# Kernel optimization log

Measured on AMD Instinct MI355X. Metric: run time of the kernel, lower is better.

## Reference

```python
import jax, jax.numpy as jnp
import numpy as np

D_MODEL = 1024
NUM_HEADS = 16
D_K = D_MODEL // NUM_HEADS  # 64


def setup_inputs() -> dict:
    key = jax.random.key(0)
    k1, k2, k3, k4, k5 = jax.random.split(key, 5)
    scale = 1.0 / np.sqrt(D_MODEL)
    x = jax.random.normal(k1, (2, 8192, D_MODEL), dtype=jnp.float32)
    W_qkv = jax.random.normal(k2, (D_MODEL, 3 * D_MODEL), dtype=jnp.float32) * scale
    b_qkv = jax.random.normal(k3, (3 * D_MODEL,), dtype=jnp.float32) * 0.01
    W_out = jax.random.normal(k4, (D_MODEL, D_MODEL), dtype=jnp.float32) * scale
    b_out = jax.random.normal(k5, (D_MODEL,), dtype=jnp.float32) * 0.01
    return {"x": x, "W_qkv": W_qkv, "b_qkv": b_qkv, "W_out": W_out, "b_out": b_out}


def reference(x, W_qkv, b_qkv, W_out, b_out):
    B, S, _ = x.shape
    # qkv: [B, S, 3*d_model] -> reshape [B, S, H, 3*d_k] (matches torch reshape:
    # head h owns contiguous slice [h*3dk:(h+1)*3dk], split into q/k/v of d_k each)
    qkv = (jnp.einsum('bsd,de->bse', x, W_qkv) + b_qkv).reshape(B, S, NUM_HEADS, 3 * D_K)
    q, k, v = qkv[..., :D_K], qkv[..., D_K:2 * D_K], qkv[..., 2 * D_K:]
    # NOTE: faithful to source — no head transpose, so matmul contracts d_k and
    # produces scores across the HEAD axis: [B, S, H, H]
    scores = jnp.einsum('bshd,bsgd->bshg', q, k) / np.sqrt(D_K)
    attn = jax.nn.softmax(scores, axis=-1)  # softmax over heads (g)
    context = jnp.einsum('bshg,bsgd->bshd', attn, v).reshape(B, S, NUM_HEADS * D_K)
    return jnp.einsum('bsd,de->bse', context, W_out) + b_out
```

## Files before the change

kernel.cpp:

```cpp
#include <hip/hip_runtime.h>
#include <hip/hip_bf16.h>

typedef short bf16x8 __attribute__((ext_vector_type(8)));
typedef float f32x4 __attribute__((ext_vector_type(4)));
typedef ushort ushort8_t __attribute__((ext_vector_type(8)));

__device__ __forceinline__ float bf2f(ushort u) {
    union { unsigned int i; float f; } c; c.i = ((unsigned int)u) << 16; return c.f;
}
__device__ __forceinline__ ushort f2bf(float f) {
    union { float f; unsigned int i; } c; c.f = f;
    unsigned int x = c.i;
    return (ushort)((x + 0x7fffu + ((x >> 16) & 1u)) >> 16);
}

#define GLOAD_LDS16(g, l) __builtin_amdgcn_global_load_lds( \
    (const __attribute__((address_space(1))) unsigned int*)(g), \
    (__attribute__((address_space(3))) unsigned int*)(l), 16, 0, 0)

__device__ __forceinline__ void transpose_cvt_body(const float* __restrict__ in,
                                                   ushort* __restrict__ out,
                                                   int K, int N, int bx, int by,
                                                   int tid, float (*tile)[33]) {
    int n0 = bx * 32, k0 = by * 32;
    int tx = tid & 31, ty = tid >> 5;
    #pragma unroll
    for (int i = 0; i < 32; i += 8)
        tile[ty + i][tx] = in[(size_t)(k0 + ty + i) * N + n0 + tx];
    __syncthreads();
    #pragma unroll
    for (int i = 0; i < 32; i += 8)
        out[(size_t)(n0 + ty + i) * K + k0 + tx] = f2bf(tile[tx][ty + i]);
}

__global__ __launch_bounds__(256) void k_prep(const float* __restrict__ x,
                                              ushort* __restrict__ xb,
                                              const float* __restrict__ Wq,
                                              ushort* __restrict__ wqkT,
                                              const float* __restrict__ Wo,
                                              ushort* __restrict__ woT) {
    __shared__ float tile[32][33];
    const int b = blockIdx.x, tid = threadIdx.x;
    if (b < 16384) {
        int i = b * 256 + tid;
        float4 v = ((const float4*)x)[i];
        ushort4 o;
        o.x = f2bf(v.x); o.y = f2bf(v.y); o.z = f2bf(v.z); o.w = f2bf(v.w);
        ((ushort4*)xb)[i] = o;
    } else if (b < 16384 + 3072) {
        int idx = b - 16384;
        transpose_cvt_body(Wq, wqkT, 1024, 3072, idx % 96, idx / 96, tid, tile);
    } else {
        int idx = b - (16384 + 3072);
        transpose_cvt_body(Wo, woT, 1024, 1024, idx & 31, idx >> 5, tid, tile);
    }
}


#define LDSA(c,kk) (lds + (c)*65536 + (kk)*16384)
#define LDSB(c,kk) (lds + (c)*65536 + 32768 + (kk)*16384)
#define STAGE_A(c,kk,col) do { \
    GLOAD_LDS16(gA0 + (col), LDSA(c,kk) + wave*1024); \
    GLOAD_LDS16(gA1 + (col), LDSA(c,kk) + 8192 + wave*1024); } while(0)
#define STAGE_B(c,kk,col) do { \
    GLOAD_LDS16(gB0 + (col), LDSB(c,kk) + wave*1024); \
    GLOAD_LDS16(gB1 + (col), LDSB(c,kk) + 8192 + wave*1024); } while(0)
#define READ_A8(c,kk) do { const char* _p = LDSA(c,kk) + aoff; \
    _Pragma("unroll") for (int m = 0; m < 8; ++m) af[m] = *(const bf16x8*)(_p + m*1024); } while(0)
#define READ_B2(c,kk,n0) do { const char* _p = LDSB(c,kk) + boff; \
    bfr[n0] = *(const bf16x8*)(_p + (n0)*1024); \
    bfr[(n0)+1] = *(const bf16x8*)(_p + ((n0)+1)*1024); } while(0)
#define MF16(n0) do { __builtin_amdgcn_s_setprio(1); \
    _Pragma("unroll") for (int m = 0; m < 8; ++m) { \
    acc[m][n0]     = __builtin_amdgcn_mfma_f32_16x16x32_bf16(af[m], bfr[n0],     acc[m][n0],     0,0,0); \
    acc[m][(n0)+1] = __builtin_amdgcn_mfma_f32_16x16x32_bf16(af[m], bfr[(n0)+1], acc[m][(n0)+1], 0,0,0); } \
    __builtin_amdgcn_s_setprio(0); } while(0)

#define BAR __builtin_amdgcn_s_barrier()
#define SB0 __builtin_amdgcn_sched_barrier(0)
#define VM10 asm volatile("s_waitcnt vmcnt(10)")
#define VM0  asm volatile("s_waitcnt vmcnt(0)")

#define PH1(reads, stage, mf, vm) do { reads; stage; mf; SB0; vm; BAR; SB0; } while(0)

#define ITERX(kb, LAST) do { \
   PH1( { READ_A8(0,0); READ_B2(0,0,0); }, STAGE_B(1,1,(kb)+96),              MF16(0), ); \
   PH1( { READ_B2(0,0,2); },               if(!(LAST)) STAGE_A(0,0,(kb)+128), MF16(2), if(LAST) VM0; else VM10 ); \
   PH1( { READ_A8(0,1); READ_B2(0,1,0); }, if(!(LAST)) STAGE_B(0,0,(kb)+128), MF16(0), ); \
   PH1( { READ_B2(0,1,2); },               if(!(LAST)) STAGE_A(0,1,(kb)+160), MF16(2), if(!(LAST)) VM10 ); \
   PH1( { READ_A8(1,0); READ_B2(1,0,0); }, if(!(LAST)) STAGE_B(0,1,(kb)+160), MF16(0), ); \
   PH1( { READ_B2(1,0,2); },               if(!(LAST)) STAGE_A(1,0,(kb)+192), MF16(2), if(!(LAST)) VM10 ); \
   PH1( { READ_A8(1,1); READ_B2(1,1,0); }, if(!(LAST)) STAGE_B(1,0,(kb)+192), MF16(0), ); \
   PH1( { READ_B2(1,1,2); },               if(!(LAST)) STAGE_A(1,1,(kb)+224), MF16(2), if(!(LAST)) VM10 ); \
} while(0)

template<bool OUT_BF16>
__global__ __launch_bounds__(512, 2) void k_gemm256(const ushort* __restrict__ A,
                                                    const ushort* __restrict__ Bt,
                                                    const float* __restrict__ bias,
                                                    void* __restrict__ Cout,
                                                    int N, int NTN) {
    __shared__ __align__(16) char lds[131072];
    const int K = 1024;
    const int tid = threadIdx.x;
    const int wave = tid >> 6, lane = tid & 63;
    const int wr = wave >> 2, wc = wave & 3;
    const int r = lane & 15, q = lane >> 4;

    const int cpx = gridDim.x >> 3, wg = blockIdx.x;
    const int swz = (wg & 7) * cpx + (wg >> 3);
    const int tm = swz / NTN, tn = swz - tm * NTN;
    const int bm = tm * 256, bn = tn * 256;

    const int srow = tid >> 2;
    const int c16l = (tid & 3) ^ ((srow >> 1) & 3);
    const ushort* gA0 = A  + (size_t)(bm + srow) * K + c16l * 8;
    const ushort* gA1 = gA0 + (size_t)128 * K;
    const ushort* gB0 = Bt + (size_t)(bn + srow) * K + c16l * 8;
    const ushort* gB1 = gB0 + (size_t)128 * K;

    const int chunkx = ((q ^ ((r >> 1) & 3)) << 4);
    const int aoff = (wr * 128 + r) * 64 + chunkx;
    const int boff = (wc * 64 + r) * 64 + chunkx;

    f32x4 acc[8][4];
    #pragma unroll
    for (int m = 0; m < 8; ++m)
        #pragma unroll
        for (int n = 0; n < 4; ++n)
            acc[m][n] = (f32x4){0.f, 0.f, 0.f, 0.f};
    bf16x8 af[8], bfr[4];

    STAGE_A(0,0,0);  STAGE_B(0,0,0);
    STAGE_A(0,1,32); STAGE_B(0,1,32);
    STAGE_A(1,0,64); STAGE_B(1,0,64);
    STAGE_A(1,1,96);
    VM10; BAR; SB0;

    #pragma unroll 1
    for (int i = 0; i < 7; ++i) { ITERX(i * 128, 0); }
    ITERX(896, 1);

    float* Cf = (float*)Cout;
    ushort* Cb = (ushort*)Cout;
    #pragma unroll
    for (int m = 0; m < 8; ++m) {
        int row0 = bm + wr * 128 + m * 16 + q * 4;
        #pragma unroll
        for (int n = 0; n < 4; ++n) {
            int col = bn + wc * 64 + n * 16 + r;
            float bv = bias[col];
            #pragma unroll
            for (int j = 0; j < 4; ++j) {
                float v = acc[m][n][j] + bv;
                if (OUT_BF16) Cb[(size_t)(row0 + j) * N + col] = f2bf(v);
                else          Cf[(size_t)(row0 + j) * N + col] = v;
            }
        }
    }
}

__global__ __launch_bounds__(256) void k_attn_mfma(const ushort* __restrict__ qkv,
                                                   ushort* __restrict__ ctx) {
    __shared__ __align__(16) ushort vlds[4][1024];
    __shared__ __align__(16) ushort olds[4][1024];
    const int w = threadIdx.x >> 6, lane = threadIdx.x & 63;
    const size_t tok = (size_t)blockIdx.x * 4 + w;
    const ushort* row = qkv + tok * 3072;
    const int r = lane & 15, g = lane >> 4;

    {
        const int c0 = lane, c1 = lane + 64;
        bf16x8 v0 = *(const bf16x8*)(row + (c0 >> 3) * 192 + 128 + (c0 & 7) * 8);
        bf16x8 v1 = *(const bf16x8*)(row + (c1 >> 3) * 192 + 128 + (c1 & 7) * 8);
        *(bf16x8*)&vlds[w][c0 * 8] = v0;
        *(bf16x8*)&vlds[w][c1 * 8] = v1;
    }

    bf16x8 ka[2], qb[2];
    #pragma unroll
    for (int c = 0; c < 2; ++c) {
        ka[c] = *(const bf16x8*)(row + r * 192 + 64 + c * 32 + g * 8);
        qb[c] = *(const bf16x8*)(row + r * 192 +      c * 32 + g * 8);
    }
    f32x4 st = (f32x4){0.f, 0.f, 0.f, 0.f};
    st = __builtin_amdgcn_mfma_f32_16x16x32_bf16(ka[0], qb[0], st, 0, 0, 0);
    st = __builtin_amdgcn_mfma_f32_16x16x32_bf16(ka[1], qb[1], st, 0, 0, 0);

    float s[4];
    #pragma unroll
    for (int j = 0; j < 4; ++j) s[j] = st[j] * 0.125f;
    float m = fmaxf(fmaxf(s[0], s[1]), fmaxf(s[2], s[3]));
    m = fmaxf(m, __shfl_xor(m, 16));
    m = fmaxf(m, __shfl_xor(m, 32));
    float p[4], sum = 0.f;
    #pragma unroll
    for (int j = 0; j < 4; ++j) { p[j] = __expf(s[j] - m); sum += p[j]; }
    sum += __shfl_xor(sum, 16);
    sum += __shfl_xor(sum, 32);
    float inv = 1.f / sum;
    #pragma unroll
    for (int j = 0; j < 4; ++j) p[j] *= inv;

    const bool gok = (g < 2);
    const int src0 = (r + 32 * g) & 63, src1 = (src0 + 16) & 63;
    bf16x8 pa;
    #pragma unroll
    for (int j = 0; j < 4; ++j) {
        float a0 = __shfl(p[j], src0, 64);
        float a1 = __shfl(p[j], src1, 64);
        pa[j]     = (short)(gok ? f2bf(a0) : (ushort)0);
        pa[4 + j] = (short)(gok ? f2bf(a1) : (ushort)0);
    }

    #pragma unroll
    for (int db = 0; db < 4; ++db) {
        bf16x8 vb;
        #pragma unroll
        for (int j = 0; j < 8; ++j) {
            int vrow = (g & 1) * 8 + j;
            ushort ve = vlds[w][vrow * 64 + db * 16 + r];
            vb[j] = (short)(gok ? ve : (ushort)0);
        }
        f32x4 o = (f32x4){0.f, 0.f, 0.f, 0.f};
        o = __builtin_amdgcn_mfma_f32_16x16x32_bf16(pa, vb, o, 0, 0, 0);
        #pragma unroll
        for (int j = 0; j < 4; ++j)
            olds[w][(4 * g + j) * 64 + db * 16 + r] = f2bf(o[j]);
    }

    {
        const int c0 = lane, c1 = lane + 64;
        bf16x8 o0 = *(const bf16x8*)&olds[w][c0 * 8];
        bf16x8 o1 = *(const bf16x8*)&olds[w][c1 * 8];
        *(bf16x8*)(ctx + tok * 1024 + c0 * 8) = o0;
        *(bf16x8*)(ctx + tok * 1024 + c1 * 8) = o1;
    }
}

extern "C" void kernel_launch(void* const* d_in, const int* in_sizes, int n_in,
                              void* d_out, int out_size, void* d_ws, size_t ws_size,
                              hipStream_t stream) {
    const float* x     = (const float*)d_in[0];
    const float* W_qkv = (const float*)d_in[1];
    const float* b_qkv = (const float*)d_in[2];
    const float* W_out = (const float*)d_in[3];
    const float* b_out = (const float*)d_in[4];

    const int M = 16384, D = 1024, N3 = 3072;

    ushort* xb   = (ushort*)d_ws;
    ushort* wqkT = xb + (size_t)M * D;
    ushort* woT  = wqkT + (size_t)N3 * D;
    ushort* qkv  = woT + (size_t)D * D;
    ushort* ctx  = xb;

    hipLaunchKernelGGL(k_prep, dim3(16384 + 3072 + 1024), dim3(256), 0, stream,
                       x, xb, W_qkv, wqkT, W_out, woT);
    hipLaunchKernelGGL((k_gemm256<true>), dim3((N3 / 256) * (M / 256)), dim3(512), 0, stream,
                       xb, wqkT, b_qkv, (void*)qkv, N3, N3 / 256);
    hipLaunchKernelGGL(k_attn_mfma, dim3(M / 4), dim3(256), 0, stream, qkv, ctx);
    hipLaunchKernelGGL((k_gemm256<false>), dim3((D / 256) * (M / 256)), dim3(512), 0, stream,
                       ctx, woT, b_out, d_out, D, D / 256);
}
```

Baseline: 189.2 us.

## Replace 4-slot hand-scheduled GEMM pipeline with simpler 3-stage K-loop

Replaces the unrolled eight-phase GEMM main loop, which used two double-buffered 64-wide K chunks and interleaved LDS reads, global-to-LDS staging and MFMA with sched barriers, with a plain 32-iteration loop over a triple-buffered 32-wide K ring. LDS use drops from 128 KB to 96 KB. Each iteration reads all fragments, issues the staging for two tiles ahead, runs 32 MFMAs and then waits and synchronises. The change trades fine-grained overlap for simplicity and a smaller LDS footprint, but it adds a barrier per 32-K step and loses the sched_barrier control over instruction ordering.

Measured after the change: 193.5 us. 2.3% more time.

```diff
diff --git a/kernel.cpp b/kernel.cpp
--- a/kernel.cpp
+++ b/kernel.cpp
@@ -57,51 +57,27 @@
 }
 
 
-#define LDSA(c,kk) (lds + (c)*65536 + (kk)*16384)
-#define LDSB(c,kk) (lds + (c)*65536 + 32768 + (kk)*16384)
-#define STAGE_A(c,kk,col) do { \
-    GLOAD_LDS16(gA0 + (col), LDSA(c,kk) + wave*1024); \
-    GLOAD_LDS16(gA1 + (col), LDSA(c,kk) + 8192 + wave*1024); } while(0)
-#define STAGE_B(c,kk,col) do { \
-    GLOAD_LDS16(gB0 + (col), LDSB(c,kk) + wave*1024); \
-    GLOAD_LDS16(gB1 + (col), LDSB(c,kk) + 8192 + wave*1024); } while(0)
-#define READ_A8(c,kk) do { const char* _p = LDSA(c,kk) + aoff; \
-    _Pragma("unroll") for (int m = 0; m < 8; ++m) af[m] = *(const bf16x8*)(_p + m*1024); } while(0)
-#define READ_B2(c,kk,n0) do { const char* _p = LDSB(c,kk) + boff; \
-    bfr[n0] = *(const bf16x8*)(_p + (n0)*1024); \
-    bfr[(n0)+1] = *(const bf16x8*)(_p + ((n0)+1)*1024); } while(0)
-#define MF16(n0) do { __builtin_amdgcn_s_setprio(1); \
-    _Pragma("unroll") for (int m = 0; m < 8; ++m) { \
-    acc[m][n0]     = __builtin_amdgcn_mfma_f32_16x16x32_bf16(af[m], bfr[n0],     acc[m][n0],     0,0,0); \
-    acc[m][(n0)+1] = __builtin_amdgcn_mfma_f32_16x16x32_bf16(af[m], bfr[(n0)+1], acc[m][(n0)+1], 0,0,0); } \
-    __builtin_amdgcn_s_setprio(0); } while(0)
+#define LDSA(c) (lds + (size_t)(c) * 32768)
+#define LDSB(c) (lds + (size_t)(c) * 32768 + 16384)
+#define STAGE_A(c,col) do { \
+    GLOAD_LDS16(gA0 + (col), LDSA(c) + wave*1024); \
+    GLOAD_LDS16(gA1 + (col), LDSA(c) + 8192 + wave*1024); } while(0)
+#define STAGE_B(c,col) do { \
+    GLOAD_LDS16(gB0 + (col), LDSB(c) + wave*1024); \
+    GLOAD_LDS16(gB1 + (col), LDSB(c) + 8192 + wave*1024); } while(0)
 
 #define BAR __builtin_amdgcn_s_barrier()
-#define SB0 __builtin_amdgcn_sched_barrier(0)
-#define VM10 asm volatile("s_waitcnt vmcnt(10)")
-#define VM0  asm volatile("s_waitcnt vmcnt(0)")
-
-#define PH1(reads, stage, mf, vm) do { reads; stage; mf; SB0; vm; BAR; SB0; } while(0)
-
-#define ITERX(kb, LAST) do { \
-   PH1( { READ_A8(0,0); READ_B2(0,0,0); }, STAGE_B(1,1,(kb)+96),              MF16(0), ); \
-   PH1( { READ_B2(0,0,2); },               if(!(LAST)) STAGE_A(0,0,(kb)+128), MF16(2), if(LAST) VM0; else VM10 ); \
-   PH1( { READ_A8(0,1); READ_B2(0,1,0); }, if(!(LAST)) STAGE_B(0,0,(kb)+128), MF16(0), ); \
-   PH1( { READ_B2(0,1,2); },               if(!(LAST)) STAGE_A(0,1,(kb)+160), MF16(2), if(!(LAST)) VM10 ); \
-   PH1( { READ_A8(1,0); READ_B2(1,0,0); }, if(!(LAST)) STAGE_B(0,1,(kb)+160), MF16(0), ); \
-   PH1( { READ_B2(1,0,2); },               if(!(LAST)) STAGE_A(1,0,(kb)+192), MF16(2), if(!(LAST)) VM10 ); \
-   PH1( { READ_A8(1,1); READ_B2(1,1,0); }, if(!(LAST)) STAGE_B(1,0,(kb)+192), MF16(0), ); \
-   PH1( { READ_B2(1,1,2); },               if(!(LAST)) STAGE_A(1,1,(kb)+224), MF16(2), if(!(LAST)) VM10 ); \
-} while(0)
+#define VM4 asm volatile("s_waitcnt vmcnt(4)")
+#define VM0 asm volatile("s_waitcnt vmcnt(0)")
 
 template<bool OUT_BF16>
-__global__ __launch_bounds__(512, 2) void k_gemm256(const ushort* __restrict__ A,
-                                                    const ushort* __restrict__ Bt,
-                                                    const float* __restrict__ bias,
-                                                    void* __restrict__ Cout,
-                                                    int N, int NTN) {
-    __shared__ __align__(16) char lds[131072];
-    const int K = 1024;
+__global__ __launch_bounds__(512, 2) void k_gemm96(const ushort* __restrict__ A,
+                                                   const ushort* __restrict__ Bt,
+                                                   const float* __restrict__ bias,
+                                                   void* __restrict__ Cout,
+                                                   int N, int NTN) {
+    __shared__ __align__(16) char lds[98304];
+    const int K = 1024, NT = 32;
     const int tid = threadIdx.x;
     const int wave = tid >> 6, lane = tid & 63;
     const int wr = wave >> 2, wc = wave & 3;
@@ -131,15 +107,32 @@
             acc[m][n] = (f32x4){0.f, 0.f, 0.f, 0.f};
     bf16x8 af[8], bfr[4];
 
-    STAGE_A(0,0,0);  STAGE_B(0,0,0);
-    STAGE_A(0,1,32); STAGE_B(0,1,32);
-    STAGE_A(1,0,64); STAGE_B(1,0,64);
-    STAGE_A(1,1,96);
-    VM10; BAR; SB0;
-
+    STAGE_A(0, 0);  STAGE_B(0, 0);
+    STAGE_A(1, 32); STAGE_B(1, 32);
+    VM4; BAR;
+
+    int ca = 0;
     #pragma unroll 1
-    for (int i = 0; i < 7; ++i) { ITERX(i * 128, 0); }
-    ITERX(896, 1);
+    for (int t = 0; t < NT; ++t) {
+        const char* pA = LDSA(ca) + aoff;
+        const char* pB = LDSB(ca) + boff;
+        #pragma unroll
+        for (int m = 0; m < 8; ++m) af[m] = *(const bf16x8*)(pA + m * 1024);
+        #pragma unroll
+        for (int n = 0; n < 4; ++n) bfr[n] = *(const bf16x8*)(pB + n * 1024);
+        int cs = ca + 2; if (cs >= 3) cs -= 3;
+        if (t < NT - 2) { STAGE_A(cs, (t + 2) * 32); STAGE_B(cs, (t + 2) * 32); }
+        __builtin_amdgcn_s_setprio(1);
+        #pragma unroll
+        for (int m = 0; m < 8; ++m)
+            #pragma unroll
+            for (int n = 0; n < 4; ++n)
+                acc[m][n] = __builtin_amdgcn_mfma_f32_16x16x32_bf16(af[m], bfr[n], acc[m][n], 0, 0, 0);
+        __builtin_amdgcn_s_setprio(0);
+        if (t < NT - 2) VM4; else if (t == NT - 2) VM0;
+        BAR;
+        ++ca; if (ca == 3) ca = 0;
+    }
 
     float* Cf = (float*)Cout;
     ushort* Cb = (ushort*)Cout;
@@ -257,9 +250,9 @@
 
     hipLaunchKernelGGL(k_prep, dim3(16384 + 3072 + 1024), dim3(256), 0, stream,
                        x, xb, W_qkv, wqkT, W_out, woT);
-    hipLaunchKernelGGL((k_gemm256<true>), dim3((N3 / 256) * (M / 256)), dim3(512), 0, stream,
+    hipLaunchKernelGGL((k_gemm96<true>), dim3((N3 / 256) * (M / 256)), dim3(512), 0, stream,
                        xb, wqkT, b_qkv, (void*)qkv, N3, N3 / 256);
     hipLaunchKernelGGL(k_attn_mfma, dim3(M / 4), dim3(256), 0, stream, qkv, ctx);
-    hipLaunchKernelGGL((k_gemm256<false>), dim3((D / 256) * (M / 256)), dim3(512), 0, stream,
+    hipLaunchKernelGGL((k_gemm96<false>), dim3((D / 256) * (M / 256)), dim3(512), 0, stream,
                        ctx, woT, b_out, d_out, D, D / 256);
 }
```

## Use 128x128 triple-buffered GEMM kernel for output projection

Applied to the files above, without the earlier changes.

Adds a 256-thread GEMM with 128x128 tiles, a three-stage LDS ring fed by direct global-to-LDS loads, and swizzled block ordering. The output projection now uses it instead of the 256x256 kernel. The aim is more blocks and better CU fill and latency hiding for the N=1024 GEMM, which had only 256 large tiles. In exchange, operands are re-read more often and there is less register-level reuse per tile.

New measurement: 195.6 us. 3.4% more time.

```diff
diff --git a/kernel.cpp b/kernel.cpp
--- a/kernel.cpp
+++ b/kernel.cpp
@@ -79,6 +79,7 @@
 #define BAR __builtin_amdgcn_s_barrier()
 #define SB0 __builtin_amdgcn_sched_barrier(0)
 #define VM10 asm volatile("s_waitcnt vmcnt(10)")
+#define VM4  asm volatile("s_waitcnt vmcnt(4)")
 #define VM0  asm volatile("s_waitcnt vmcnt(0)")
 
 #define PH1(reads, stage, mf, vm) do { reads; stage; mf; SB0; vm; BAR; SB0; } while(0)
@@ -160,6 +161,99 @@
     }
 }
 
+
+#define LDS2A(c) (lds + (size_t)(c) * 16384)
+#define LDS2B(c) (lds + (size_t)(c) * 16384 + 8192)
+#define STAGE2_A(c,col) do { \
+    GLOAD_LDS16(gA0 + (col), LDS2A(c) + wave*1024); \
+    GLOAD_LDS16(gA1 + (col), LDS2A(c) + 4096 + wave*1024); } while(0)
+#define STAGE2_B(c,col) do { \
+    GLOAD_LDS16(gB0 + (col), LDS2B(c) + wave*1024); \
+    GLOAD_LDS16(gB1 + (col), LDS2B(c) + 4096 + wave*1024); } while(0)
+
+template<bool OUT_BF16>
+__global__ __launch_bounds__(256, 3) void k_gemm128(const ushort* __restrict__ A,
+                                                    const ushort* __restrict__ Bt,
+                                                    const float* __restrict__ bias,
+                                                    void* __restrict__ Cout,
+                                                    int N, int NTN) {
+    __shared__ __align__(16) char lds[49152];
+    const int K = 1024, NT = 32;
+    const int tid = threadIdx.x;
+    const int wave = tid >> 6, lane = tid & 63;
+    const int wr = wave >> 1, wc = wave & 1;
+    const int r = lane & 15, q = lane >> 4;
+
+    const int cpx = gridDim.x >> 3, wg = blockIdx.x;
+    const int swz = (wg & 7) * cpx + (wg >> 3);
+    const int tm = swz / NTN, tn = swz - tm * NTN;
+    const int bm = tm * 128, bn = tn * 128;
+
+    const int srow = tid >> 2;
+    const int c16l = (tid & 3) ^ ((srow >> 1) & 3);
+    const ushort* gA0 = A  + (size_t)(bm + srow) * K + c16l * 8;
+    const ushort* gA1 = gA0 + (size_t)64 * K;
+    const ushort* gB0 = Bt + (size_t)(bn + srow) * K + c16l * 8;
+    const ushort* gB1 = gB0 + (size_t)64 * K;
+
+    const int chunkx = ((q ^ ((r >> 1) & 3)) << 4);
+    const int aoff = (wr * 64 + r) * 64 + chunkx;
+    const int boff = (wc * 64 + r) * 64 + chunkx;
+
+    f32x4 acc[4][4];
+    #pragma unroll
+    for (int m = 0; m < 4; ++m)
+        #pragma unroll
+        for (int n = 0; n < 4; ++n)
+            acc[m][n] = (f32x4){0.f, 0.f, 0.f, 0.f};
+    bf16x8 af[4], bfr[4];
+
+    STAGE2_A(0, 0);  STAGE2_B(0, 0);
+    STAGE2_A(1, 32); STAGE2_B(1, 32);
+    VM4; BAR;
+
+    int ca = 0;
+    #pragma unroll 1
+    for (int t = 0; t < NT; ++t) {
+        const char* pA = LDS2A(ca) + aoff;
+        const char* pB = LDS2B(ca) + boff;
+        #pragma unroll
+        for (int m = 0; m < 4; ++m) af[m] = *(const bf16x8*)(pA + m * 1024);
+        #pragma unroll
+        for (int n = 0; n < 4; ++n) bfr[n] = *(const bf16x8*)(pB + n * 1024);
+        int cs = ca + 2; if (cs >= 3) cs -= 3;
+        if (t < NT - 2) { STAGE2_A(cs, (t + 2) * 32); STAGE2_B(cs, (t + 2) * 32); }
+        __builtin_amdgcn_s_setprio(1);
+        #pragma unroll
+        for (int m = 0; m < 4; ++m)
+            #pragma unroll
+            for (int n = 0; n < 4; ++n)
+                acc[m][n] = __builtin_amdgcn_mfma_f32_16x16x32_bf16(af[m], bfr[n], acc[m][n], 0, 0, 0);
+        __builtin_amdgcn_s_setprio(0);
+        if (t < NT - 2) VM4; else if (t == NT - 2) VM0;
+        BAR;
+        ++ca; if (ca == 3) ca = 0;
+    }
+
+    float* Cf = (float*)Cout;
+    ushort* Cb = (ushort*)Cout;
+    #pragma unroll
+    for (int m = 0; m < 4; ++m) {
+        int row0 = bm + wr * 64 + m * 16 + q * 4;
+        #pragma unroll
+        for (int n = 0; n < 4; ++n) {
+            int col = bn + wc * 64 + n * 16 + r;
+            float bv = bias[col];
+            #pragma unroll
+            for (int j = 0; j < 4; ++j) {
+                float v = acc[m][n][j] + bv;
+                if (OUT_BF16) Cb[(size_t)(row0 + j) * N + col] = f2bf(v);
+                else          Cf[(size_t)(row0 + j) * N + col] = v;
+            }
+        }
+    }
+}
+
 __global__ __launch_bounds__(256) void k_attn_mfma(const ushort* __restrict__ qkv,
                                                    ushort* __restrict__ ctx) {
     __shared__ __align__(16) ushort vlds[4][1024];
@@ -260,6 +354,6 @@
     hipLaunchKernelGGL((k_gemm256<true>), dim3((N3 / 256) * (M / 256)), dim3(512), 0, stream,
                        xb, wqkT, b_qkv, (void*)qkv, N3, N3 / 256);
     hipLaunchKernelGGL(k_attn_mfma, dim3(M / 4), dim3(256), 0, stream, qkv, ctx);
-    hipLaunchKernelGGL((k_gemm256<false>), dim3((D / 256) * (M / 256)), dim3(512), 0, stream,
-                       ctx, woT, b_out, d_out, D, D / 256);
-}
+    hipLaunchKernelGGL((k_gemm128<false>), dim3((D / 128) * (M / 128)), dim3(256), 0, stream,
+                       ctx, woT, b_out, d_out, D, D / 128);
+}
```
